# Kernel tuning notes

Hardware: AMD Instinct MI355X
Metric: run time of the kernel (lower is better)

Reference implementation:

```python
import jax, jax.numpy as jnp
import numpy as np

N_DIM = 768
HIDDEN_DIM = 768
BATCH = 4
SEQ = 2048


def setup_inputs() -> dict:
    key = jax.random.key(0)
    ks = jax.random.split(key, 9)
    s_in = 1.0 / np.sqrt(N_DIM)
    s_h = 1.0 / np.sqrt(HIDDEN_DIM)
    return {
        "x": jax.random.normal(ks[0], (BATCH, SEQ, N_DIM), dtype=jnp.float32),
        # torch Linear weights: [out_features, in_features]
        "wq": jax.random.uniform(ks[1], (HIDDEN_DIM, N_DIM), jnp.float32, -s_in, s_in),
        "bq": jax.random.uniform(ks[2], (HIDDEN_DIM,), jnp.float32, -s_in, s_in),
        "wk": jax.random.uniform(ks[3], (HIDDEN_DIM, N_DIM), jnp.float32, -s_in, s_in),
        "bk": jax.random.uniform(ks[4], (HIDDEN_DIM,), jnp.float32, -s_in, s_in),
        "wv": jax.random.uniform(ks[5], (HIDDEN_DIM, N_DIM), jnp.float32, -s_in, s_in),
        "bv": jax.random.uniform(ks[6], (HIDDEN_DIM,), jnp.float32, -s_in, s_in),
        "wo": jax.random.uniform(ks[7], (N_DIM, HIDDEN_DIM), jnp.float32, -s_h, s_h),
        "bo": jax.random.uniform(ks[8], (N_DIM,), jnp.float32, -s_h, s_h),
    }


def reference(x, wq, bq, wk, bk, wv, bv, wo, bo):
    # q,k,v: [B, S, H]
    q = jnp.einsum("bsd,hd->bsh", x, wq) + bq
    k = jnp.einsum("bsd,hd->bsh", x, wk) + bk
    v = jnp.einsum("bsd,hd->bsh", x, wv) + bv
    # NOTE: faithful to source — no 1/sqrt(d) scaling, no mask.
    scores = jnp.einsum("bqh,bkh->bqk", q, k)  # [B, S, S]
    attn = jax.nn.softmax(scores, axis=-1)
    y = jnp.einsum("bqk,bkh->bqh", attn, v)  # [B, S, H]
    out = jnp.einsum("bsh,dh->bsd", y, wo) + bo
    return out
```

## Files before the change

### kernel.cpp

```cpp
#include <hip/hip_runtime.h>

typedef _Float16 f16;
typedef _Float16 f16x8 __attribute__((ext_vector_type(8)));
typedef float f32x4 __attribute__((ext_vector_type(4)));

#define GLD16(g, l) __builtin_amdgcn_global_load_lds( \
    (const __attribute__((address_space(1))) void*)(g), \
    (__attribute__((address_space(3))) void*)(l), 16, 0, 0)

template <typename OutT, int BM, int BN, int MODE, int MINW>
__global__ __launch_bounds__(256, MINW)
void gemm_kernel(const f16* __restrict__ A, long sA,
                 const f16* __restrict__ B, long sB,
                 void* __restrict__ Cv, long sC,
                 void* __restrict__ C2v,
                 const float* __restrict__ bias,
                 const float* __restrict__ bias2,
                 int N, int K)
{
    constexpr int FM = BM / 32;
    constexpr int FN = BN / 32;
    constexpr int IA = BM / 32;
    constexpr int IB = BN / 32;

    OutT* C  = (OutT*)Cv;
    OutT* C2 = (OutT*)C2v;
    const int tid  = threadIdx.x;
    const int wave = tid >> 6;
    const int lane = tid & 63;
    const int bz   = blockIdx.z;
    A += (long)bz * sA;
    B += (long)bz * sB;
    C += (long)bz * sC;
    const long bm = (long)blockIdx.x * BM;
    const long bn = (long)blockIdx.y * BN;

    __shared__ f16 sAt[BM * 64];
    __shared__ f16 sBt[BN * 64];

    const int srow = lane >> 3;
    const int gch  = ((lane & 7) ^ srow) * 8;

    const f16* gAb = A + (bm + wave * (BM / 4) + srow) * (long)K + gch;
    const f16* gBb = B + (bn + wave * (BN / 4) + srow) * (long)K + gch;

    const int wm = (wave >> 1) * (BM / 2);
    const int wn = (wave & 1) * (BN / 2);
    const int lr = lane & 15;
    const int qd = lane >> 4;
    const int swz0 = ((0 * 4 + qd) ^ (lr & 7)) * 8;
    const int swz1 = ((1 * 4 + qd) ^ (lr & 7)) * 8;

    f32x4 acc[FM][FN] = {};

    for (int k0 = 0; k0 < K; k0 += 64) {
        #pragma unroll
        for (int i = 0; i < IA; ++i)
            GLD16(gAb + k0 + (long)i * 8 * K, &sAt[(wave * (BM / 4) + i * 8) * 64]);
        #pragma unroll
        for (int i = 0; i < IB; ++i)
            GLD16(gBb + k0 + (long)i * 8 * K, &sBt[(wave * (BN / 4) + i * 8) * 64]);
        __syncthreads();

        #pragma unroll
        for (int h = 0; h < 2; ++h) {
            const int swz = h ? swz1 : swz0;
            f16x8 af[FM], bf[FN];
            #pragma unroll
            for (int t = 0; t < FM; ++t)
                af[t] = *(const f16x8*)&sAt[(wm + t * 16 + lr) * 64 + swz];
            #pragma unroll
            for (int t = 0; t < FN; ++t)
                bf[t] = *(const f16x8*)&sBt[(wn + t * 16 + lr) * 64 + swz];
            #pragma unroll
            for (int tm = 0; tm < FM; ++tm)
                #pragma unroll
                for (int tn = 0; tn < FN; ++tn)
                    acc[tm][tn] = __builtin_amdgcn_mfma_f32_16x16x32_f16(
                        af[tm], bf[tn], acc[tm][tn], 0, 0, 0);
        }
        __syncthreads();
    }

    #pragma unroll
    for (int tn = 0; tn < FN; ++tn) {
        const long col = bn + wn + tn * 16 + lr;
        OutT* dst = C;
        long cc = col, stride = N;
        float bc = 0.f;
        if (MODE == 1) bc = bias[col];
        if (MODE == 3) {
            stride = 768;
            if (col >= 768) { dst = C2; cc = col - 768; bc = bias2[cc]; }
            else            { bc = bias[cc]; }
        }
        #pragma unroll
        for (int tm = 0; tm < FM; ++tm) {
            #pragma unroll
            for (int r = 0; r < 4; ++r) {
                const long row = bm + wm + tm * 16 + qd * 4 + r;
                float v = acc[tm][tn][r] + bc;
                if (MODE == 2) v += bias[row];
                dst[row * stride + cc] = (OutT)v;
            }
        }
    }
}

__global__ __launch_bounds__(256)
void softmax_kernel(f16* __restrict__ S)
{
    const long row = blockIdx.x;
    f16* p = S + row * 2048;
    const int tid  = threadIdx.x;
    const int wave = tid >> 6;
    const int lane = tid & 63;

    f16x8 x = *(const f16x8*)&p[tid * 8];
    float v[8];
    float m = -1e30f;
    #pragma unroll
    for (int j = 0; j < 8; ++j) { v[j] = (float)x[j]; m = fmaxf(m, v[j]); }
    #pragma unroll
    for (int off = 32; off > 0; off >>= 1) m = fmaxf(m, __shfl_down(m, off));

    __shared__ float rm[4], rs[4];
    if (lane == 0) rm[wave] = m;
    __syncthreads();
    m = fmaxf(fmaxf(rm[0], rm[1]), fmaxf(rm[2], rm[3]));

    float s = 0.f;
    #pragma unroll
    for (int j = 0; j < 8; ++j) { v[j] = __expf(v[j] - m); s += v[j]; }
    #pragma unroll
    for (int off = 32; off > 0; off >>= 1) s += __shfl_down(s, off);
    if (lane == 0) rs[wave] = s;
    __syncthreads();
    s = rs[0] + rs[1] + rs[2] + rs[3];
    const float inv = 1.0f / s;

    f16x8 y;
    #pragma unroll
    for (int j = 0; j < 8; ++j) y[j] = (f16)(v[j] * inv);
    *(f16x8*)&p[tid * 8] = y;
}

__global__ __launch_bounds__(256)
void cvt_all_kernel(const float* __restrict__ x,
                    const float* __restrict__ w0, const float* __restrict__ w1,
                    const float* __restrict__ w2, const float* __restrict__ w3,
                    f16* __restrict__ x16, f16* __restrict__ w16)
{
    const float* in; f16* out; long i;
    if (blockIdx.x < 3072) {
        in = x; out = x16;
        i = ((long)blockIdx.x * 256 + threadIdx.x) * 8;
    } else {
        const int wb  = blockIdx.x - 3072;
        const int sel = wb / 288;
        in  = (sel == 0) ? w0 : (sel == 1) ? w1 : (sel == 2) ? w2 : w3;
        out = w16 + (long)sel * 589824;
        i = ((long)(wb - sel * 288) * 256 + threadIdx.x) * 8;
    }
    float4 a = *(const float4*)(in + i);
    float4 b = *(const float4*)(in + i + 4);
    f16x8 o;
    o[0] = (f16)a.x; o[1] = (f16)a.y; o[2] = (f16)a.z; o[3] = (f16)a.w;
    o[4] = (f16)b.x; o[5] = (f16)b.y; o[6] = (f16)b.z; o[7] = (f16)b.w;
    *(f16x8*)&out[i] = o;
}

extern "C" void kernel_launch(void* const* d_in, const int* in_sizes, int n_in,
                              void* d_out, int out_size, void* d_ws, size_t ws_size,
                              hipStream_t stream)
{
    const float* x  = (const float*)d_in[0];
    const float* wq = (const float*)d_in[1];
    const float* bq = (const float*)d_in[2];
    const float* wk = (const float*)d_in[3];
    const float* bk = (const float*)d_in[4];
    const float* wv = (const float*)d_in[5];
    const float* bv = (const float*)d_in[6];
    const float* wo = (const float*)d_in[7];
    const float* bo = (const float*)d_in[8];

    char* ws = (char*)d_ws;
    f16* x16 = (f16*)(ws + 0);
    f16* w16 = (f16*)(ws + 12582912);
    f16* Q   = (f16*)(ws + 17301504);
    f16* Kb  = (f16*)(ws + 29884416);
    f16* VT  = (f16*)(ws + 42467328);
    f16* S   = (f16*)(ws + 55050240);
    f16* Y   = (f16*)(ws + 88604672);

    f16* wv16 = w16 + 2 * 589824;
    f16* wo16 = w16 + 3 * 589824;

    cvt_all_kernel<<<4224, 256, 0, stream>>>(x, wq, wk, wv, wo, x16, w16);

    gemm_kernel<f16, 128, 128, 3, 3><<<dim3(64, 12, 1), 256, 0, stream>>>(
        x16, 0, w16, 0, Q, 0, Kb, bq, bk, 1536, 768);
    gemm_kernel<f16, 64, 128, 2, 4><<<dim3(12, 16, 4), 256, 0, stream>>>(
        wv16, 0, x16, (long)2048 * 768, VT, (long)768 * 2048, nullptr,
        bv, nullptr, 2048, 768);
    gemm_kernel<f16, 128, 128, 0, 3><<<dim3(16, 16, 4), 256, 0, stream>>>(
        Q, (long)2048 * 768, Kb, (long)2048 * 768, S, (long)2048 * 2048,
        nullptr, nullptr, nullptr, 2048, 768);
    softmax_kernel<<<8192, 256, 0, stream>>>(S);
    gemm_kernel<f16, 64, 128, 0, 4><<<dim3(32, 6, 4), 256, 0, stream>>>(
        S, (long)2048 * 2048, VT, (long)768 * 2048, Y, (long)2048 * 768,
        nullptr, nullptr, nullptr, 768, 2048);
    gemm_kernel<float, 64, 128, 1, 4><<<dim3(128, 6, 1), 256, 0, stream>>>(
        Y, 0, wo16, 0, (float*)d_out, 0, nullptr, bo, nullptr, 768, 768);
}
```

Baseline: 235.9 us.

## Add double-buffered LDS pipeline to GEMM and retune tile shapes

```diff
diff --git a/kernel.cpp b/kernel.cpp
--- a/kernel.cpp
+++ b/kernel.cpp
@@ -8,7 +8,9 @@
     (const __attribute__((address_space(1))) void*)(g), \
     (__attribute__((address_space(3))) void*)(l), 16, 0, 0)
 
-template <typename OutT, int BM, int BN, int MODE, int MINW>
+#define MEMFENCE asm volatile("" ::: "memory")
+
+template <typename OutT, int BM, int BN, int MODE, int MINW, int DBUF>
 __global__ __launch_bounds__(256, MINW)
 void gemm_kernel(const f16* __restrict__ A, long sA,
                  const f16* __restrict__ B, long sB,
@@ -35,8 +37,8 @@
     const long bm = (long)blockIdx.x * BM;
     const long bn = (long)blockIdx.y * BN;
 
-    __shared__ f16 sAt[BM * 64];
-    __shared__ f16 sBt[BN * 64];
+    __shared__ f16 sAt[(DBUF + 1) * BM * 64];
+    __shared__ f16 sBt[(DBUF + 1) * BN * 64];
 
     const int srow = lane >> 3;
     const int gch  = ((lane & 7) ^ srow) * 8;
@@ -53,25 +55,30 @@
 
     f32x4 acc[FM][FN] = {};
 
-    for (int k0 = 0; k0 < K; k0 += 64) {
+    auto issue = [&](int k0, int b) {
+        f16* dA = &sAt[b * BM * 64];
+        f16* dB = &sBt[b * BN * 64];
         #pragma unroll
         for (int i = 0; i < IA; ++i)
-            GLD16(gAb + k0 + (long)i * 8 * K, &sAt[(wave * (BM / 4) + i * 8) * 64]);
+            GLD16(gAb + k0 + (long)i * 8 * K, &dA[(wave * (BM / 4) + i * 8) * 64]);
         #pragma unroll
         for (int i = 0; i < IB; ++i)
-            GLD16(gBb + k0 + (long)i * 8 * K, &sBt[(wave * (BN / 4) + i * 8) * 64]);
-        __syncthreads();
-
+            GLD16(gBb + k0 + (long)i * 8 * K, &dB[(wave * (BN / 4) + i * 8) * 64]);
+    };
+
+    auto compute = [&](int b) {
+        const f16* dA = &sAt[b * BM * 64];
+        const f16* dB = &sBt[b * BN * 64];
         #pragma unroll
         for (int h = 0; h < 2; ++h) {
             const int swz = h ? swz1 : swz0;
             f16x8 af[FM], bf[FN];
             #pragma unroll
             for (int t = 0; t < FM; ++t)
-                af[t] = *(const f16x8*)&sAt[(wm + t * 16 + lr) * 64 + swz];
+                af[t] = *(const f16x8*)&dA[(wm + t * 16 + lr) * 64 + swz];
             #pragma unroll
             for (int t = 0; t < FN; ++t)
-                bf[t] = *(const f16x8*)&sBt[(wn + t * 16 + lr) * 64 + swz];
+                bf[t] = *(const f16x8*)&dB[(wn + t * 16 + lr) * 64 + swz];
             #pragma unroll
             for (int tm = 0; tm < FM; ++tm)
                 #pragma unroll
@@ -79,7 +86,26 @@
                     acc[tm][tn] = __builtin_amdgcn_mfma_f32_16x16x32_f16(
                         af[tm], bf[tn], acc[tm][tn], 0, 0, 0);
         }
+    };
+
+    if (DBUF) {
+        const int NS = K >> 6;
+        issue(0, 0);
         __syncthreads();
+        for (int s = 0; s < NS; ++s) {
+            MEMFENCE;
+            if (s + 1 < NS) issue((s + 1) * 64, (s + 1) & 1);
+            MEMFENCE;
+            compute(s & 1);
+            __syncthreads();
+        }
+    } else {
+        for (int k0 = 0; k0 < K; k0 += 64) {
+            issue(k0, 0);
+            __syncthreads();
+            compute(0);
+            __syncthreads();
+        }
     }
 
     #pragma unroll
@@ -198,18 +224,18 @@
 
     cvt_all_kernel<<<4224, 256, 0, stream>>>(x, wq, wk, wv, wo, x16, w16);
 
-    gemm_kernel<f16, 128, 128, 3, 3><<<dim3(64, 12, 1), 256, 0, stream>>>(
+    gemm_kernel<f16, 128, 128, 3, 3, 0><<<dim3(64, 12, 1), 256, 0, stream>>>(
         x16, 0, w16, 0, Q, 0, Kb, bq, bk, 1536, 768);
-    gemm_kernel<f16, 64, 128, 2, 4><<<dim3(12, 16, 4), 256, 0, stream>>>(
+    gemm_kernel<f16, 64, 128, 2, 3, 1><<<dim3(12, 16, 4), 256, 0, stream>>>(
         wv16, 0, x16, (long)2048 * 768, VT, (long)768 * 2048, nullptr,
         bv, nullptr, 2048, 768);
-    gemm_kernel<f16, 128, 128, 0, 3><<<dim3(16, 16, 4), 256, 0, stream>>>(
+    gemm_kernel<f16, 128, 256, 0, 2, 0><<<dim3(16, 8, 4), 256, 0, stream>>>(
         Q, (long)2048 * 768, Kb, (long)2048 * 768, S, (long)2048 * 2048,
         nullptr, nullptr, nullptr, 2048, 768);
     softmax_kernel<<<8192, 256, 0, stream>>>(S);
-    gemm_kernel<f16, 64, 128, 0, 4><<<dim3(32, 6, 4), 256, 0, stream>>>(
+    gemm_kernel<f16, 128, 64, 0, 3, 1><<<dim3(16, 12, 4), 256, 0, stream>>>(
         S, (long)2048 * 2048, VT, (long)768 * 2048, Y, (long)2048 * 768,
         nullptr, nullptr, nullptr, 768, 2048);
-    gemm_kernel<float, 64, 128, 1, 4><<<dim3(128, 6, 1), 256, 0, stream>>>(
+    gemm_kernel<float, 128, 64, 1, 3, 1><<<dim3(64, 12, 1), 256, 0, stream>>>(
         Y, 0, wo16, 0, (float*)d_out, 0, nullptr, bo, nullptr, 768, 768);
 }
```

New measurement: 232.0 us. Within noise of the previous version (-1.7%).
